# Kernel optimization log

Measured on AMD Instinct MI355X. Metric: run time of the kernel, lower is better.

Reference implementation:

```python
import jax, jax.numpy as jnp
import numpy as np

EPS = 1e-5

def _bn_relu(h, gamma, beta):
    # h: (b, c, n); BatchNorm1d in training mode: stats over (batch, spatial)
    mean = jnp.mean(h, axis=(0, 2), keepdims=True)
    var = jnp.var(h, axis=(0, 2), keepdims=True)
    h = (h - mean) * jax.lax.rsqrt(var + EPS)
    h = h * gamma[None, :, None] + beta[None, :, None]
    return jax.nn.relu(h)

def setup_inputs() -> dict:
    key = jax.random.key(0)
    ks = jax.random.split(key, 8)
    b, c, n, k, N = 4, 128, 4096, 32, 16384
    x = jax.random.normal(ks[0], (b, c, n, k), dtype=jnp.float32)
    group_idx = jax.random.randint(ks[1], (b, n, k), 0, N, dtype=jnp.int64)
    fps_idx = jax.random.randint(ks[2], (b, n), 0, N, dtype=jnp.int64)
    w1 = jax.random.normal(ks[3], (c, 2 * c), dtype=jnp.float32) * (1.0 / np.sqrt(2 * c))
    b1 = jnp.zeros((c,), dtype=jnp.float32)
    g1 = jnp.ones((c,), dtype=jnp.float32)
    be1 = jnp.zeros((c,), dtype=jnp.float32)
    w2 = jax.random.normal(ks[4], (c, c), dtype=jnp.float32) * (1.0 / np.sqrt(c))
    b2 = jnp.zeros((c,), dtype=jnp.float32)
    g2 = jnp.ones((c,), dtype=jnp.float32)
    be2 = jnp.zeros((c,), dtype=jnp.float32)
    return {"x": x, "group_idx": group_idx, "fps_idx": fps_idx, "N": N,
            "w1": w1, "b1": b1, "g1": g1, "be1": be1,
            "w2": w2, "b2": b2, "g2": g2, "be2": be2}

def reference(x, group_idx, fps_idx, N, w1, b1, g1, be1, w2, b2, g2, be2):
    b, c, n, k = x.shape
    # local max pool over neighbors: (b, c, n)
    group_x = jnp.max(x, axis=-1)
    # scatter_max of (b, n*k, c) into (b, N, c), out initialized to zeros
    dil = jnp.transpose(x, (0, 2, 3, 1)).reshape(b * n * k, c)
    idx = group_idx.reshape(b, n * k) + (jnp.arange(b, dtype=group_idx.dtype) * N)[:, None]
    seg = jax.ops.segment_max(dil, idx.reshape(-1), num_segments=b * N)
    # torch scatter_max with zero-initialized out: max with 0, empty segs -> 0
    seg = jnp.maximum(seg, 0.0).reshape(b, N, c)
    # gather FPS-sampled points: (b, n, c) -> (b, c, n)
    gathered = jnp.take_along_axis(seg, fps_idx[:, :, None], axis=1)
    dilated_x = jnp.transpose(gathered, (0, 2, 1))
    feat = jnp.concatenate([group_x, dilated_x], axis=1)  # (b, 2c, n)
    h = jnp.einsum('oc,bcn->bon', w1, feat) + b1[None, :, None]
    h = _bn_relu(h, g1, be1)
    h = jnp.einsum('oc,bcn->bon', w2, h) + b2[None, :, None]
    h = _bn_relu(h, g2, be2)
    return h
```

## Files before the change

kernel.cpp:

```cpp
#include <hip/hip_runtime.h>

constexpr int Bb = 4, Cc = 128, Nn = 4096, Kk = 32, Ns = 16384;
constexpr int ROWS = Bb * Nn;
constexpr int NK = Nn * Kk;
constexpr int NPART = 256;
constexpr int QOFF = NPART * 128;
constexpr float EPS = 1e-5f;

typedef __attribute__((ext_vector_type(8))) short short8;
typedef __attribute__((ext_vector_type(4))) float f32x4;

__device__ __forceinline__ unsigned short f2bf(float f) {
    unsigned int u = __float_as_uint(f);
    unsigned int r = u + 0x7FFFu + ((u >> 16) & 1u);
    return (unsigned short)(r >> 16);
}

constexpr size_t SZ_SEG   = (size_t)Bb * Ns * Cc * 4;
constexpr size_t OFF_SEG  = 0;
constexpr size_t SZ_GX    = (size_t)ROWS * Cc * 4;
constexpr size_t OFF_GX   = OFF_SEG + SZ_SEG;
constexpr size_t OFF_H1   = OFF_GX + SZ_GX;
constexpr size_t OFF_H2   = OFF_H1 + SZ_GX;
constexpr size_t SZ_PART  = (size_t)NPART * 128 * 2 * 4;
constexpr size_t OFF_P1   = OFF_H2 + SZ_GX;
constexpr size_t OFF_P2   = OFF_P1 + SZ_PART;
constexpr size_t OFF_FLAG = OFF_P2 + SZ_PART;

__global__ __launch_bounds__(256) void k_prep(const int* __restrict__ fps,
                                              float4* __restrict__ seg4,
                                              int* __restrict__ flags) {
    int i = blockIdx.x * 32 + (threadIdx.x >> 3);
    int lane = threadIdx.x & 7;
    int bb = i >> 12;
    int fi = fps[i];
    if (lane == 0) flags[bb * Ns + fi] = i;
    float4 z{0.f, 0.f, 0.f, 0.f};
    size_t base = ((size_t)bb * Ns + fi) * 32 + lane;
    seg4[base + 0] = z; seg4[base + 8] = z;
    seg4[base + 16] = z; seg4[base + 24] = z;
}

__global__ __launch_bounds__(256) void k_scatter(
        const float* __restrict__ x, const int* __restrict__ gidx,
        const int* __restrict__ flags, const int* __restrict__ fps,
        float* __restrict__ gx, unsigned int* __restrict__ seg) {
    int nn = blockIdx.x, bb = blockIdx.y;
    int t = threadIdx.x;
    __shared__ float tile[128][33];
    __shared__ float gbuf[128];
    __shared__ unsigned int srow[32];
    __shared__ int klist[32];
    __shared__ int nflag;
    __shared__ unsigned int fmask;

    if (t == 0) { nflag = 0; fmask = 0u; }
    __syncthreads();
    if (t < 32) {
        int idxv = gidx[((bb * Nn + nn) << 5) + t];
        srow[t] = (unsigned int)(bb * Ns + idxv) * 128u;
        int fl = flags[bb * Ns + idxv];
        int j = fl & 16383;
        if (((j >> 12) == bb) && (fps[j] == idxv)) {
            int pos = atomicAdd(&nflag, 1);
            klist[pos] = t;
            atomicOr(&fmask, 1u << t);
        }
    }

    int k4 = (t & 7) * 4;
    int cq = t >> 3;
    const float* xb = x + (size_t)bb * Cc * NK + (size_t)nn * Kk;
    float4 v[4];
    #pragma unroll
    for (int p = 0; p < 4; p++)
        v[p] = *(const float4*)(xb + (size_t)(cq + p * 32) * NK + k4);

    __syncthreads();
    unsigned int mask = fmask;
    bool f0 = (mask >> (k4 + 0)) & 1, f1 = (mask >> (k4 + 1)) & 1;
    bool f2 = (mask >> (k4 + 2)) & 1, f3 = (mask >> (k4 + 3)) & 1;

    #pragma unroll
    for (int p = 0; p < 4; p++) {
        int ch = cq + p * 32;
        float4 w = v[p];
        float m = fmaxf(fmaxf(w.x, w.y), fmaxf(w.z, w.w));
        m = fmaxf(m, __shfl_xor(m, 1, 64));
        m = fmaxf(m, __shfl_xor(m, 2, 64));
        m = fmaxf(m, __shfl_xor(m, 4, 64));
        if ((t & 7) == 0) gbuf[ch] = m;
        if (f0) tile[ch][k4 + 0] = w.x;
        if (f1) tile[ch][k4 + 1] = w.y;
        if (f2) tile[ch][k4 + 2] = w.z;
        if (f3) tile[ch][k4 + 3] = w.w;
    }
    __syncthreads();

    if (t < 128) gx[((size_t)(bb * Nn + nn)) * 128 + t] = gbuf[t];

    int nf = nflag;
    int ch = t & 127, rep = t >> 7;
    for (int it = rep; it < nf; it += 2) {
        int k = klist[it];
        float val = tile[ch][k];
        if (val > 0.f) atomicMax(seg + srow[k] + ch, __float_as_uint(val));
    }
}

__global__ __launch_bounds__(512) void k_gemm1(
        const float* __restrict__ gx, const float* __restrict__ segf,
        const int* __restrict__ fps, const float* __restrict__ w1,
        const float* __restrict__ b1, float* __restrict__ h1,
        float* __restrict__ part) {
    __shared__ __align__(16) unsigned short A_lds[64][72];
    __shared__ __align__(16) unsigned short B_lds[64][72];
    __shared__ float reds[8][32], redq[8][32];
    __shared__ int rowbase[64];
    int t = threadIdx.x;
    int rt = blockIdx.x >> 1;
    int m0 = rt * 64;
    int c0g = (blockIdx.x & 1) * 64;
    if (t < 64) rowbase[t] = (((m0 + t) >> 12) * Ns + fps[m0 + t]) * 128;
    int w = t >> 6, l = t & 63;
    int r0 = (w >> 1) * 16, c0 = (w & 1) * 32;
    int lr = l & 15, lk = (l >> 4) * 8;
    f32x4 acc[2] = {};
    for (int k0 = 0; k0 < 256; k0 += 64) {
        __syncthreads();
        #pragma unroll
        for (int i = 0; i < 2; i++) {
            int q = t + i * 512;
            int row = q >> 4, kq = (q & 15) * 4;
            int k = k0 + kq;
            float4 v;
            if (k0 < 128) v = *(const float4*)(gx + (size_t)(m0 + row) * 128 + k);
            else          v = *(const float4*)(segf + rowbase[row] + (k - 128));
            ushort4 o{f2bf(v.x), f2bf(v.y), f2bf(v.z), f2bf(v.w)};
            *(ushort4*)&A_lds[row][kq] = o;
        }
        #pragma unroll
        for (int i = 0; i < 2; i++) {
            int q = t + i * 512;
            int col = q >> 4, kq = (q & 15) * 4;
            float4 v = *(const float4*)(w1 + (size_t)(c0g + col) * 256 + k0 + kq);
            ushort4 o{f2bf(v.x), f2bf(v.y), f2bf(v.z), f2bf(v.w)};
            *(ushort4*)&B_lds[col][kq] = o;
        }
        __syncthreads();
        #pragma unroll
        for (int ks = 0; ks < 2; ks++) {
            short8 a = *(const short8*)&A_lds[r0 + lr][ks * 32 + lk];
            #pragma unroll
            for (int cb = 0; cb < 2; cb++) {
                short8 b = *(const short8*)&B_lds[c0 + cb * 16 + lr][ks * 32 + lk];
                acc[cb] = __builtin_amdgcn_mfma_f32_16x16x32_bf16(a, b, acc[cb], 0, 0, 0);
            }
        }
    }
    int orow = m0 + r0 + (l >> 4) * 4;
    #pragma unroll
    for (int cb = 0; cb < 2; cb++) {
        int lc = c0 + cb * 16 + lr;
        int col = c0g + lc;
        float bias = b1[col];
        float sv = 0.f, qv = 0.f;
        #pragma unroll
        for (int r = 0; r < 4; r++) {
            float o = acc[cb][r] + bias;
            h1[(size_t)(orow + r) * 128 + col] = o;
            sv += o; qv += o * o;
        }
        sv += __shfl_xor(sv, 16, 64); sv += __shfl_xor(sv, 32, 64);
        qv += __shfl_xor(qv, 16, 64); qv += __shfl_xor(qv, 32, 64);
        if (l < 16) { reds[w][cb * 16 + l] = sv; redq[w][cb * 16 + l] = qv; }
    }
    __syncthreads();
    if (t < 64) {
        int par = t >> 5, o = t & 31;
        float s = reds[par][o] + reds[par + 2][o] + reds[par + 4][o] + reds[par + 6][o];
        float q = redq[par][o] + redq[par + 2][o] + redq[par + 4][o] + redq[par + 6][o];
        part[rt * 128 + c0g + t] = s;
        part[QOFF + rt * 128 + c0g + t] = q;
    }
}

__global__ __launch_bounds__(512) void k_gemm2(
        const float* __restrict__ h1, const float* __restrict__ part1,
        const float* __restrict__ g1, const float* __restrict__ be1,
        const float* __restrict__ w2, const float* __restrict__ b2,
        float* __restrict__ h2, float* __restrict__ part2) {
    __shared__ __align__(16) unsigned short A_lds[64][72];
    __shared__ __align__(16) unsigned short B_lds[64][72];
    __shared__ float reds[8][32], redq[8][32];
    __shared__ float ssc[128], ssh[128], tmp[256];
    int t = threadIdx.x;
    int rt = blockIdx.x >> 1;
    int m0 = rt * 64;
    int c0g = (blockIdx.x & 1) * 64;
    if (t < 256) {
        int ch = t & 127;
        const float* src = part1 + (t >> 7) * QOFF + ch;
        float a = 0.f;
        #pragma unroll 8
        for (int j = 0; j < NPART; j++) a += src[j * 128];
        tmp[t] = a;
    }
    __syncthreads();
    if (t < 128) {
        float mean = tmp[t] * (1.0f / 16384.0f);
        float var = tmp[t + 128] * (1.0f / 16384.0f) - mean * mean;
        float sc = g1[t] * rsqrtf(var + EPS);
        ssc[t] = sc;
        ssh[t] = be1[t] - mean * sc;
    }
    __syncthreads();
    int w = t >> 6, l = t & 63;
    int r0 = (w >> 1) * 16, c0 = (w & 1) * 32;
    int lr = l & 15, lk = (l >> 4) * 8;
    f32x4 acc[2] = {};
    for (int k0 = 0; k0 < 128; k0 += 64) {
        __syncthreads();
        #pragma unroll
        for (int i = 0; i < 2; i++) {
            int q = t + i * 512;
            int row = q >> 4, kq = (q & 15) * 4;
            int k = k0 + kq;
            float4 v = *(const float4*)(h1 + (size_t)(m0 + row) * 128 + k);
            float a0 = fmaxf(0.f, fmaf(v.x, ssc[k + 0], ssh[k + 0]));
            float a1 = fmaxf(0.f, fmaf(v.y, ssc[k + 1], ssh[k + 1]));
            float a2 = fmaxf(0.f, fmaf(v.z, ssc[k + 2], ssh[k + 2]));
            float a3 = fmaxf(0.f, fmaf(v.w, ssc[k + 3], ssh[k + 3]));
            ushort4 o{f2bf(a0), f2bf(a1), f2bf(a2), f2bf(a3)};
            *(ushort4*)&A_lds[row][kq] = o;
        }
        #pragma unroll
        for (int i = 0; i < 2; i++) {
            int q = t + i * 512;
            int col = q >> 4, kq = (q & 15) * 4;
            float4 v = *(const float4*)(w2 + (size_t)(c0g + col) * 128 + k0 + kq);
            ushort4 o{f2bf(v.x), f2bf(v.y), f2bf(v.z), f2bf(v.w)};
            *(ushort4*)&B_lds[col][kq] = o;
        }
        __syncthreads();
        #pragma unroll
        for (int ks = 0; ks < 2; ks++) {
            short8 a = *(const short8*)&A_lds[r0 + lr][ks * 32 + lk];
            #pragma unroll
            for (int cb = 0; cb < 2; cb++) {
                short8 b = *(const short8*)&B_lds[c0 + cb * 16 + lr][ks * 32 + lk];
                acc[cb] = __builtin_amdgcn_mfma_f32_16x16x32_bf16(a, b, acc[cb], 0, 0, 0);
            }
        }
    }
    int orow = m0 + r0 + (l >> 4) * 4;
    #pragma unroll
    for (int cb = 0; cb < 2; cb++) {
        int lc = c0 + cb * 16 + lr;
        int col = c0g + lc;
        float bias = b2[col];
        float sv = 0.f, qv = 0.f;
        #pragma unroll
        for (int r = 0; r < 4; r++) {
            float o = acc[cb][r] + bias;
            h2[(size_t)(orow + r) * 128 + col] = o;
            sv += o; qv += o * o;
        }
        sv += __shfl_xor(sv, 16, 64); sv += __shfl_xor(sv, 32, 64);
        qv += __shfl_xor(qv, 16, 64); qv += __shfl_xor(qv, 32, 64);
        if (l < 16) { reds[w][cb * 16 + l] = sv; redq[w][cb * 16 + l] = qv; }
    }
    __syncthreads();
    if (t < 64) {
        int par = t >> 5, o = t & 31;
        float s = reds[par][o] + reds[par + 2][o] + reds[par + 4][o] + reds[par + 6][o];
        float q = redq[par][o] + redq[par + 2][o] + redq[par + 4][o] + redq[par + 6][o];
        part2[rt * 128 + c0g + t] = s;
        part2[QOFF + rt * 128 + c0g + t] = q;
    }
}

__global__ __launch_bounds__(512) void k_out(const float* __restrict__ h2,
                                             const float* __restrict__ part2,
                                             const float* __restrict__ g2,
                                             const float* __restrict__ be2,
                                             float* __restrict__ out) {
    __shared__ float tile[64][129];
    __shared__ float lsc[128], lsh[128], tmp[256];
    int t = threadIdx.x;
    int bb = blockIdx.y, n0 = blockIdx.x * 64;
    if (t < 256) {
        int ch = t & 127;
        const float* src = part2 + (t >> 7) * QOFF + ch;
        float a = 0.f;
        #pragma unroll 8
        for (int j = 0; j < NPART; j++) a += src[j * 128];
        tmp[t] = a;
    }
    __syncthreads();
    if (t < 128) {
        float mean = tmp[t] * (1.0f / 16384.0f);
        float var = tmp[t + 128] * (1.0f / 16384.0f) - mean * mean;
        float sc = g2[t] * rsqrtf(var + EPS);
        lsc[t] = sc;
        lsh[t] = be2[t] - mean * sc;
    }
    #pragma unroll
    for (int i = 0; i < 4; i++) {
        int fq = t + i * 512;
        int row = fq >> 5;
        int c4 = (fq & 31) * 4;
        float4 v = *(const float4*)(h2 + ((size_t)(bb * Nn + n0 + row)) * 128 + c4);
        tile[row][c4 + 0] = v.x; tile[row][c4 + 1] = v.y;
        tile[row][c4 + 2] = v.z; tile[row][c4 + 3] = v.w;
    }
    __syncthreads();
    int j = t & 63, og = t >> 6;
    #pragma unroll
    for (int o = og; o < 128; o += 8) {
        float v = fmaxf(0.f, fmaf(tile[j][o], lsc[o], lsh[o]));
        out[((size_t)(bb * 128 + o)) * Nn + n0 + j] = v;
    }
}

extern "C" void kernel_launch(void* const* d_in, const int* in_sizes, int n_in,
                              void* d_out, int out_size, void* d_ws, size_t ws_size,
                              hipStream_t stream) {
    const float* x    = (const float*)d_in[0];
    const int*   gidx = (const int*)d_in[1];
    const int*   fps  = (const int*)d_in[2];
    const float* w1   = (const float*)d_in[4];
    const float* b1   = (const float*)d_in[5];
    const float* g1   = (const float*)d_in[6];
    const float* be1  = (const float*)d_in[7];
    const float* w2   = (const float*)d_in[8];
    const float* b2   = (const float*)d_in[9];
    const float* g2   = (const float*)d_in[10];
    const float* be2  = (const float*)d_in[11];
    float* out = (float*)d_out;

    char* ws = (char*)d_ws;
    unsigned int* seg  = (unsigned int*)(ws + OFF_SEG);
    float* segf        = (float*)(ws + OFF_SEG);
    float4* seg4       = (float4*)(ws + OFF_SEG);
    float* gx          = (float*)(ws + OFF_GX);
    float* h1          = (float*)(ws + OFF_H1);
    float* h2          = (float*)(ws + OFF_H2);
    float* part1       = (float*)(ws + OFF_P1);
    float* part2       = (float*)(ws + OFF_P2);
    int* flags         = (int*)(ws + OFF_FLAG);

    k_prep<<<ROWS / 32, 256, 0, stream>>>(fps, seg4, flags);
    k_scatter<<<dim3(Nn, Bb), 256, 0, stream>>>(x, gidx, flags, fps, gx, seg);
    k_gemm1<<<ROWS / 32, 512, 0, stream>>>(gx, segf, fps, w1, b1, h1, part1);
    k_gemm2<<<ROWS / 32, 512, 0, stream>>>(h1, part1, g1, be1, w2, b2, h2, part2);
    k_out<<<dim3(Nn / 64, Bb), 512, 0, stream>>>(h2, part2, g2, be2, out);
}
```

Baseline: 121.8 us.

## Replace atomicMax segment scatter with per-segment contributor lists and gather kernel

Removes the zeroed segment buffer and the per-channel float atomicMax scatter. Each sampled segment now keeps a capped list of contributing (point, neighbor) entries, built with one atomicAdd per contributor, and the contributing feature vectors are written to a staging array. A new gather kernel reduces those entries per channel into a dense gathered tensor, which the first GEMM reads contiguously. This adds an extra kernel launch and extra memory traffic for the staged values, plus a slow linear-scan fallback whenever a segment has more than CAP contributors.

```diff
diff --git a/kernel.cpp b/kernel.cpp
--- a/kernel.cpp
+++ b/kernel.cpp
@@ -5,6 +5,7 @@
 constexpr int NK = Nn * Kk;
 constexpr int NPART = 256;
 constexpr int QOFF = NPART * 128;
+constexpr int CAP = 32;
 constexpr float EPS = 1e-5f;
 
 typedef __attribute__((ext_vector_type(8))) short short8;
@@ -16,40 +17,39 @@
     return (unsigned short)(r >> 16);
 }
 
-constexpr size_t SZ_SEG   = (size_t)Bb * Ns * Cc * 4;
-constexpr size_t OFF_SEG  = 0;
+constexpr size_t OFF_GX   = 0;
 constexpr size_t SZ_GX    = (size_t)ROWS * Cc * 4;
-constexpr size_t OFF_GX   = OFF_SEG + SZ_SEG;
-constexpr size_t OFF_H1   = OFF_GX + SZ_GX;
+constexpr size_t OFF_GDIL = OFF_GX + SZ_GX;
+constexpr size_t OFF_H1   = OFF_GDIL + SZ_GX;
 constexpr size_t OFF_H2   = OFF_H1 + SZ_GX;
 constexpr size_t SZ_PART  = (size_t)NPART * 128 * 2 * 4;
 constexpr size_t OFF_P1   = OFF_H2 + SZ_GX;
 constexpr size_t OFF_P2   = OFF_P1 + SZ_PART;
 constexpr size_t OFF_FLAG = OFF_P2 + SZ_PART;
+constexpr size_t OFF_CNT  = OFF_FLAG + (size_t)Bb * Ns * 4;
+constexpr size_t OFF_LIST = OFF_CNT + (size_t)Bb * Ns * 4;
+constexpr size_t OFF_VAL  = OFF_LIST + (size_t)Bb * Ns * CAP * 4;
 
 __global__ __launch_bounds__(256) void k_prep(const int* __restrict__ fps,
-                                              float4* __restrict__ seg4,
-                                              int* __restrict__ flags) {
-    int i = blockIdx.x * 32 + (threadIdx.x >> 3);
-    int lane = threadIdx.x & 7;
-    int bb = i >> 12;
-    int fi = fps[i];
-    if (lane == 0) flags[bb * Ns + fi] = i;
-    float4 z{0.f, 0.f, 0.f, 0.f};
-    size_t base = ((size_t)bb * Ns + fi) * 32 + lane;
-    seg4[base + 0] = z; seg4[base + 8] = z;
-    seg4[base + 16] = z; seg4[base + 24] = z;
+                                              int* __restrict__ flags,
+                                              unsigned int* __restrict__ cnt) {
+    int t = blockIdx.x * 256 + threadIdx.x;
+    cnt[t] = 0u;
+    if (t < ROWS) {
+        int bb = t >> 12;
+        flags[bb * Ns + fps[t]] = t;
+    }
 }
 
 __global__ __launch_bounds__(256) void k_scatter(
         const float* __restrict__ x, const int* __restrict__ gidx,
         const int* __restrict__ flags, const int* __restrict__ fps,
-        float* __restrict__ gx, unsigned int* __restrict__ seg) {
+        unsigned int* __restrict__ cnt, int* __restrict__ list,
+        float* __restrict__ gx, float* __restrict__ val) {
     int nn = blockIdx.x, bb = blockIdx.y;
     int t = threadIdx.x;
     __shared__ float tile[128][33];
     __shared__ float gbuf[128];
-    __shared__ unsigned int srow[32];
     __shared__ int klist[32];
     __shared__ int nflag;
     __shared__ unsigned int fmask;
@@ -58,13 +58,15 @@
     __syncthreads();
     if (t < 32) {
         int idxv = gidx[((bb * Nn + nn) << 5) + t];
-        srow[t] = (unsigned int)(bb * Ns + idxv) * 128u;
         int fl = flags[bb * Ns + idxv];
         int j = fl & 16383;
         if (((j >> 12) == bb) && (fps[j] == idxv)) {
             int pos = atomicAdd(&nflag, 1);
             klist[pos] = t;
             atomicOr(&fmask, 1u << t);
+            unsigned int slot = atomicAdd(&cnt[bb * Ns + idxv], 1u);
+            if (slot < (unsigned)CAP)
+                list[((size_t)bb * Ns + idxv) * CAP + slot] = (nn << 5) | t;
         }
     }
 
@@ -103,25 +105,49 @@
     int ch = t & 127, rep = t >> 7;
     for (int it = rep; it < nf; it += 2) {
         int k = klist[it];
-        float val = tile[ch][k];
-        if (val > 0.f) atomicMax(seg + srow[k] + ch, __float_as_uint(val));
-    }
+        val[((size_t)bb * NK + (nn << 5) + k) * 128 + ch] = tile[ch][k];
+    }
+}
+
+__global__ __launch_bounds__(256) void k_gather(
+        const int* __restrict__ fps, const unsigned int* __restrict__ cnt,
+        const int* __restrict__ list, const float* __restrict__ val,
+        const int* __restrict__ gidx, float* __restrict__ gdil) {
+    __shared__ int ent[2][CAP];
+    int t = threadIdx.x;
+    int half = t >> 7, ch = t & 127;
+    int row = blockIdx.x * 2 + half;
+    int bb = row >> 12;
+    int sg = fps[row];
+    unsigned int m = cnt[bb * Ns + sg];
+    int mm = (int)(m < (unsigned)CAP ? m : (unsigned)CAP);
+    if (ch < mm) ent[half][ch] = list[((size_t)bb * Ns + sg) * CAP + ch];
+    __syncthreads();
+    float acc = 0.f;
+    if (m <= (unsigned)CAP) {
+        #pragma unroll 4
+        for (int e = 0; e < mm; e++)
+            acc = fmaxf(acc, val[((size_t)bb * NK + ent[half][e]) * 128 + ch]);
+    } else {
+        const int* gj = gidx + (size_t)bb * NK;
+        for (int e = 0; e < NK; e++)
+            if (gj[e] == sg)
+                acc = fmaxf(acc, val[((size_t)bb * NK + e) * 128 + ch]);
+    }
+    gdil[(size_t)row * 128 + ch] = acc;
 }
 
 __global__ __launch_bounds__(512) void k_gemm1(
-        const float* __restrict__ gx, const float* __restrict__ segf,
-        const int* __restrict__ fps, const float* __restrict__ w1,
-        const float* __restrict__ b1, float* __restrict__ h1,
-        float* __restrict__ part) {
+        const float* __restrict__ gx, const float* __restrict__ gdil,
+        const float* __restrict__ w1, const float* __restrict__ b1,
+        float* __restrict__ h1, float* __restrict__ part) {
     __shared__ __align__(16) unsigned short A_lds[64][72];
     __shared__ __align__(16) unsigned short B_lds[64][72];
     __shared__ float reds[8][32], redq[8][32];
-    __shared__ int rowbase[64];
     int t = threadIdx.x;
     int rt = blockIdx.x >> 1;
     int m0 = rt * 64;
     int c0g = (blockIdx.x & 1) * 64;
-    if (t < 64) rowbase[t] = (((m0 + t) >> 12) * Ns + fps[m0 + t]) * 128;
     int w = t >> 6, l = t & 63;
     int r0 = (w >> 1) * 16, c0 = (w & 1) * 32;
     int lr = l & 15, lk = (l >> 4) * 8;
@@ -135,7 +161,7 @@
             int k = k0 + kq;
             float4 v;
             if (k0 < 128) v = *(const float4*)(gx + (size_t)(m0 + row) * 128 + k);
-            else          v = *(const float4*)(segf + rowbase[row] + (k - 128));
+            else          v = *(const float4*)(gdil + (size_t)(m0 + row) * 128 + (k - 128));
             ushort4 o{f2bf(v.x), f2bf(v.y), f2bf(v.z), f2bf(v.w)};
             *(ushort4*)&A_lds[row][kq] = o;
         }
@@ -340,19 +366,21 @@
     float* out = (float*)d_out;
 
     char* ws = (char*)d_ws;
-    unsigned int* seg  = (unsigned int*)(ws + OFF_SEG);
-    float* segf        = (float*)(ws + OFF_SEG);
-    float4* seg4       = (float4*)(ws + OFF_SEG);
     float* gx          = (float*)(ws + OFF_GX);
+    float* gdil        = (float*)(ws + OFF_GDIL);
     float* h1          = (float*)(ws + OFF_H1);
     float* h2          = (float*)(ws + OFF_H2);
     float* part1       = (float*)(ws + OFF_P1);
     float* part2       = (float*)(ws + OFF_P2);
     int* flags         = (int*)(ws + OFF_FLAG);
-
-    k_prep<<<ROWS / 32, 256, 0, stream>>>(fps, seg4, flags);
-    k_scatter<<<dim3(Nn, Bb), 256, 0, stream>>>(x, gidx, flags, fps, gx, seg);
-    k_gemm1<<<ROWS / 32, 512, 0, stream>>>(gx, segf, fps, w1, b1, h1, part1);
+    unsigned int* cnt  = (unsigned int*)(ws + OFF_CNT);
+    int* list          = (int*)(ws + OFF_LIST);
+    float* val         = (float*)(ws + OFF_VAL);
+
+    k_prep<<<256, 256, 0, stream>>>(fps, flags, cnt);
+    k_scatter<<<dim3(Nn, Bb), 256, 0, stream>>>(x, gidx, flags, fps, cnt, list, gx, val);
+    k_gather<<<ROWS / 2, 256, 0, stream>>>(fps, cnt, list, val, gidx, gdil);
+    k_gemm1<<<ROWS / 32, 512, 0, stream>>>(gx, gdil, w1, b1, h1, part1);
     k_gemm2<<<ROWS / 32, 512, 0, stream>>>(h1, part1, g1, be1, w2, b2, h2, part2);
     k_out<<<dim3(Nn / 64, Bb), 512, 0, stream>>>(h2, part2, g2, be2, out);
 }
```

New measurement: 150.0 us. 23.2% more time.
